# Kernel tuning notes

Measured on AMD Instinct MI355X. Metric: run time of the kernel, lower is better.

The kernel has to match this reference:

```python
import jax, jax.numpy as jnp
import numpy as np

T = 15
L = 10.0
LAM = 0.1
RHO = 1.0
NUM_CONV_A = 32
NUM_CONV_B = 32
DICT_DIM = 7
STRIDE_A = 1
STRIDE_B = 1
DN = ('NCHW', 'OIHW', 'NCHW')


def _fro_normalize(W):
    # normalize each (d, d) filter slice by its Frobenius norm (torch F.normalize, p='fro', dim=(-1,-2))
    n = jnp.sqrt(jnp.sum(W * W, axis=(-1, -2), keepdims=True))
    return W / jnp.maximum(n, 1e-12)


def _conv(y, W, s):
    # torch F.conv2d(y, W, stride=s), VALID padding
    return jax.lax.conv_general_dilated(y, W, (s, s), 'VALID', dimension_numbers=DN)


def _convT(x, W, s):
    # torch F.conv_transpose2d(x, W, stride=s); W in forward-conv layout (O, I, kh, kw)
    return jax.lax.conv_transpose(x, W, (s, s), 'VALID', dimension_numbers=DN, transpose_kernel=True)


def setup_inputs() -> dict:
    key = jax.random.key(0)
    ky, ka, kb = jax.random.split(key, 3)
    y = jax.random.normal(ky, (16, 1, 256, 256), dtype=jnp.float32)
    A = _fro_normalize(jax.random.normal(ka, (NUM_CONV_A, 1, DICT_DIM, DICT_DIM), dtype=jnp.float32))
    B = _fro_normalize(jax.random.normal(kb, (NUM_CONV_B, 1, DICT_DIM, DICT_DIM), dtype=jnp.float32))
    return {'y': y, 'A': A, 'B': B}


def reference(y, A, B):
    n, _, H, W = y.shape
    Dx = (H - DICT_DIM) // STRIDE_A + 1
    Du = (H - DICT_DIM) // STRIDE_B + 1
    Dx2 = (W - DICT_DIM) // STRIDE_A + 1
    Du2 = (W - DICT_DIM) // STRIDE_B + 1
    x0 = jnp.zeros((n, NUM_CONV_A, Dx, Dx2), dtype=y.dtype)
    u0 = jnp.zeros((n, NUM_CONV_B, Du, Du2), dtype=y.dtype)

    def step(carry, _):
        x_old, x_tmp, u_old, u_tmp, t_old = carry
        Ax = _convT((1.0 + 1.0 / RHO) * x_tmp, A, STRIDE_A)
        Bu = _convT(u_tmp, B, STRIDE_B)
        res = y - (Ax + Bu)
        x_new = x_tmp + _conv(res, A, STRIDE_A) / L
        u_new = u_tmp + _conv(res, B, STRIDE_B) / L
        # twosided soft-threshold
        u_new = jax.nn.relu(jnp.abs(u_new) - LAM / L) * jnp.sign(u_new)
        t_new = (1.0 + jnp.sqrt(1.0 + 4.0 * t_old * t_old)) / 2.0
        c = (t_old - 1.0) / t_new
        x_tmp2 = x_new + c * (x_new - x_old)
        u_tmp2 = u_new + c * (u_new - u_old)
        return (x_new, x_tmp2, u_new, u_tmp2, t_new), None

    init = (x0, x0, u0, u0, jnp.float32(1.0))
    (x_new, _, u_new, _, _), _ = jax.lax.scan(step, init, None, length=T)

    Ax_hat = _convT(x_new, A, STRIDE_A)
    Bu_hat = _convT(u_new, B, STRIDE_B)
    y_hat = Ax_hat + Bu_hat
    return y_hat, x_new, u_new, Ax_hat, Bu_hat
```

## Files before the change

### kernel.cpp

```cpp
#include <hip/hip_runtime.h>
#include <cmath>

#define NB 16
#define CC 32
#define HH 256
#define WW 256
#define DD 250
#define ALPHA 2.0f
#define INVL 0.1f
#define THR 0.01f

#define IMG_SZ (HH*WW)
#define IMG_TOT (NB*IMG_SZ)
#define FLD_SZ (DD*DD)
#define FLD_TOT ((size_t)NB*CC*FLD_SZ)

#define SRS 264
#define LRS 260

__device__ __forceinline__ float rfl(float x) {
    return __int_as_float(__builtin_amdgcn_readfirstlane(__float_as_int(x)));
}
__device__ __forceinline__ float sthr(float v) {
    float a = fabsf(v) - THR; a = a > 0.f ? a : 0.f;
    return (v > 0.f) ? a : ((v < 0.f) ? -a : 0.f);
}

#define CONV_ROW(ACC, Aa) do { \
    _Pragma("unroll") \
    for (int b = 0; b < 7; ++b) { \
        const float wv = wt[Aa][b]; \
        ACC.x += wv*win[b+0]; ACC.y += wv*win[b+1]; \
        ACC.z += wv*win[b+2]; ACC.w += wv*win[b+3]; \
    } } while (0)

#define GATH_ROW(ACC, Aa) do { \
    _Pragma("unroll") \
    for (int b = 0; b < 7; ++b) { \
        const float wv = wt[Aa][b]; \
        ACC.x += wv*win[8-b+0]; ACC.y += wv*win[8-b+1]; \
        ACC.z += wv*win[8-b+2]; ACC.w += wv*win[8-b+3]; \
    } } while (0)

__global__ __launch_bounds__(512) void k_step(
    const float* __restrict__ rin,
    const float* su_cur, float* su_on,
    float* __restrict__ Xinc, float* __restrict__ Uacc,
    const float* __restrict__ Afil, const float* __restrict__ Bfil,
    float cmom, int first)
{
    __shared__ __align__(16) float resT[22*SRS];
    __shared__ __align__(16) float stile[2][16*SRS];

    const int p0  = blockIdx.x * 16;
    const int f   = blockIdx.y;
    const int n   = blockIdx.z;
    const int tid = threadIdx.x;
    const bool isx = (f == 0);

    {
        float4 z = make_float4(0.f,0.f,0.f,0.f);
        float4* sp = (float4*)&stile[0][0];
        for (int i = tid; i < 2*16*SRS/4; i += 512) sp[i] = z;
    }
    {
        const float* rb = rin + (size_t)n * IMG_SZ;
        for (int i = tid; i < 22*66; i += 512) {
            int r  = i / 66;
            int c4 = (i - r*66) << 2;
            int gr = p0 + r;
            float4 v = make_float4(0.f,0.f,0.f,0.f);
            if (gr < HH && c4 < WW) v = *(const float4*)(rb + gr*WW + c4);
            *(float4*)&resT[r*SRS + c4] = v;
        }
    }
    __syncthreads();

    const int rg  = tid >> 6;
    const int q4  = (tid & 63) << 2;
    const bool qok = (q4 <= 248);
    const int p_0 = p0 + 2*rg;

    const float* Wb = isx ? Afil : Bfil;
    float* img = (isx ? Xinc : Uacc) + (size_t)n * IMG_SZ;

    const bool momentum = (!isx) && (!first) && (cmom != 0.f);
    const bool plain    = (!isx) && (!first) && (cmom == 0.f);

    float4 ia0 = make_float4(0.f,0.f,0.f,0.f), ia1 = ia0, ia2 = ia0;

    const size_t fbase = (size_t)n * CC * FLD_SZ;
    const bool r0ok = qok && (p_0     < DD);
    const bool r1ok = qok && (p_0 + 1 < DD);
    const size_t off0 = fbase + (size_t)p_0*DD + q4;
    const size_t off1 = off0 + DD;

    for (int c = 0; c < CC; ++c) {
        float wt[7][7];
        {
            const float* Wp = Wb + c*49;
#pragma unroll
            for (int a = 0; a < 7; ++a)
#pragma unroll
                for (int b = 0; b < 7; ++b)
                    wt[a][b] = rfl(Wp[a*7 + b]);
        }

        const size_t co = (size_t)c * FLD_SZ;
        float4 sc0 = make_float4(0.f,0.f,0.f,0.f), sc1 = sc0, so0 = sc0, so1 = sc0;
        if (momentum) {
            if (r0ok) { sc0 = *(const float4*)(su_cur + co + off0);
                        so0 = *(const float4*)(su_on  + co + off0); }
            if (r1ok) { sc1 = *(const float4*)(su_cur + co + off1);
                        so1 = *(const float4*)(su_on  + co + off1); }
        } else if (plain) {
            if (r0ok) sc0 = *(const float4*)(su_cur + co + off0);
            if (r1ok) sc1 = *(const float4*)(su_cur + co + off1);
        }

        float4 a0 = make_float4(0.f,0.f,0.f,0.f), a1 = a0;
#pragma unroll
        for (int rr = 0; rr < 8; ++rr) {
            const float* lp = &resT[(2*rg + rr)*SRS + q4];
            float4 A0 = *(const float4*)lp;
            float4 A1 = *(const float4*)(lp + 4);
            float4 A2 = *(const float4*)(lp + 8);
            const float win[12] = {A0.x,A0.y,A0.z,A0.w, A1.x,A1.y,A1.z,A1.w,
                                   A2.x,A2.y,A2.z,A2.w};
            if (rr <= 6) CONV_ROW(a0, rr);
            if (rr >= 1) CONV_ROW(a1, rr-1);
        }

        float4 o0 = make_float4(a0.x*INVL, a0.y*INVL, a0.z*INVL, a0.w*INVL);
        float4 o1 = make_float4(a1.x*INVL, a1.y*INVL, a1.z*INVL, a1.w*INVL);
        if (momentum) {
            o0.x += sc0.x + cmom*(sc0.x - so0.x);
            o0.y += sc0.y + cmom*(sc0.y - so0.y);
            o0.z += sc0.z + cmom*(sc0.z - so0.z);
            o0.w += sc0.w + cmom*(sc0.w - so0.w);
            o1.x += sc1.x + cmom*(sc1.x - so1.x);
            o1.y += sc1.y + cmom*(sc1.y - so1.y);
            o1.z += sc1.z + cmom*(sc1.z - so1.z);
            o1.w += sc1.w + cmom*(sc1.w - so1.w);
        } else if (plain) {
            o0.x += sc0.x; o0.y += sc0.y; o0.z += sc0.z; o0.w += sc0.w;
            o1.x += sc1.x; o1.y += sc1.y; o1.z += sc1.z; o1.w += sc1.w;
        }
        if (!isx) {
            o0.x = sthr(o0.x); o0.y = sthr(o0.y); o0.z = sthr(o0.z); o0.w = sthr(o0.w);
            o1.x = sthr(o1.x); o1.y = sthr(o1.y); o1.z = sthr(o1.z); o1.w = sthr(o1.w);
        }

        const int bb = c & 1;
        if (r0ok) {
            if (!isx) {
                float* dst = su_on + co + off0;
                if (q4 <= 244) *(float4*)dst = o0;
                else           *(float2*)dst = make_float2(o0.x, o0.y);
            }
            float* d0 = &stile[bb][(2*rg)*SRS + q4 + 8];
            if (q4 <= 244) *(float4*)d0 = o0;
            else           *(float2*)d0 = make_float2(o0.x, o0.y);
        }
        if (r1ok) {
            if (!isx) {
                float* dst = su_on + co + off1;
                if (q4 <= 244) *(float4*)dst = o1;
                else           *(float2*)dst = make_float2(o1.x, o1.y);
            }
            float* d1 = &stile[bb][(2*rg + 1)*SRS + q4 + 8];
            if (q4 <= 244) *(float4*)d1 = o1;
            else           *(float2*)d1 = make_float2(o1.x, o1.y);
        }
        __syncthreads();
#pragma unroll
        for (int k9 = 0; k9 < 9; ++k9) {
            const int k = 3*rg - 6 + k9;
            if (k >= 0 && k < 16) {
                const float* sp = &stile[bb][k*SRS + q4];
                float4 B0 = *(const float4*)sp;
                float4 B1 = *(const float4*)(sp + 4);
                float4 B2 = *(const float4*)(sp + 8);
                const float win[12] = {B0.x,B0.y,B0.z,B0.w, B1.x,B1.y,B1.z,B1.w,
                                       B2.x,B2.y,B2.z,B2.w};
                if (k9 <= 6)            GATH_ROW(ia0, 6 - k9);
                if (k9 >= 1 && k9 <= 7) GATH_ROW(ia1, 7 - k9);
                if (k9 >= 2)            GATH_ROW(ia2, 8 - k9);
            }
        }
    }

#pragma unroll
    for (int d = 0; d < 3; ++d) {
        const int h = 3*rg + d;
        if (h < 22) {
            const int habs = p0 + h;
            if (habs < HH) {
                float4 v = (d == 0) ? ia0 : (d == 1) ? ia1 : ia2;
                float* ip = img + (size_t)habs*WW + q4;
                if (h >= 6 && h <= 15) {
                    *(float4*)ip = v;
                } else {
                    atomicAdd(ip + 0, v.x);
                    atomicAdd(ip + 1, v.y);
                    atomicAdd(ip + 2, v.z);
                    atomicAdd(ip + 3, v.w);
                }
            }
        }
    }
}

__global__ __launch_bounds__(256) void k_res(
    const float* __restrict__ y,
    float* Xinc, float* Uacc,
    const float* __restrict__ XAv,
    float* XBv,
    float* Uc,
    float* __restrict__ resb, float* __restrict__ Racc,
    float cb, float cm, float alf)
{
    int i = blockIdx.x*256 + threadIdx.x;
    if (i >= IMG_TOT/4) return;
    float4 z = make_float4(0.f,0.f,0.f,0.f);

    float4 xi = ((const float4*)Xinc)[i];  ((float4*)Xinc)[i] = z;
    float4 ua = ((const float4*)Uacc)[i];  ((float4*)Uacc)[i] = z;
    float4 xa = ((const float4*)XAv)[i];

    float4 xt;
    if (cb != 0.f) {
        float4 xb = ((const float4*)XBv)[i];
        const float cbp = 1.f + cb;
        xt.x = cbp*xa.x - cb*xb.x + xi.x;
        xt.y = cbp*xa.y - cb*xb.y + xi.y;
        xt.z = cbp*xa.z - cb*xb.z + xi.z;
        xt.w = cbp*xa.w - cb*xb.w + xi.w;
    } else {
        xt.x = xa.x + xi.x; xt.y = xa.y + xi.y;
        xt.z = xa.z + xi.z; xt.w = xa.w + xi.w;
    }
    ((float4*)XBv)[i] = xt;

    float4 ucp = z;
    if (cm != 0.f) ucp = ((const float4*)Uc)[i];
    ((float4*)Uc)[i] = ua;

    float4 yv = ((const float4*)y)[i];
    const float cp = 1.f + cm;
    float4 r;
    r.x = yv.x - ALPHA*(cp*xt.x - cm*xa.x) - (cp*ua.x - cm*ucp.x);
    r.y = yv.y - ALPHA*(cp*xt.y - cm*xa.y) - (cp*ua.y - cm*ucp.y);
    r.z = yv.z - ALPHA*(cp*xt.z - cm*xa.z) - (cp*ua.z - cm*ucp.z);
    r.w = yv.w - ALPHA*(cp*xt.w - cm*xa.w) - (cp*ua.w - cm*ucp.w);
    ((float4*)resb)[i] = r;

    float4 ra = ((const float4*)Racc)[i];
    ra.x += alf*r.x; ra.y += alf*r.y; ra.z += alf*r.z; ra.w += alf*r.w;
    ((float4*)Racc)[i] = ra;
}

__global__ __launch_bounds__(256) void k_xfield(
    const float* __restrict__ Racc, const float* __restrict__ yimg,
    float* __restrict__ xout, const float* __restrict__ Afil, float alf0)
{
    __shared__ float lr[22*LRS + 8];

    const int c   = blockIdx.x;
    const int p0  = blockIdx.y * 16;
    const int n   = blockIdx.z;
    const int tid = threadIdx.x;

    const float* rb = Racc + (size_t)n * IMG_SZ;
    const float* yb = yimg + (size_t)n * IMG_SZ;
#pragma unroll
    for (int it = 0; it < 6; ++it) {
        int idx = tid + it*256;
        if (idx < 22*64) {
            int r = idx >> 6, c4 = (idx & 63) << 2;
            int gr = p0 + r;
            float4 v = make_float4(0.f,0.f,0.f,0.f);
            if (gr < HH) {
                float4 a = *(const float4*)(rb + gr*WW + c4);
                float4 b = *(const float4*)(yb + gr*WW + c4);
                v.x = a.x + alf0*b.x; v.y = a.y + alf0*b.y;
                v.z = a.z + alf0*b.z; v.w = a.w + alf0*b.w;
            }
            *(float4*)&lr[r*LRS + c4] = v;
        }
    }
    if (tid < 8) lr[22*LRS + tid] = 0.f;

    float wt[7][7];
    {
        const float* Wp = Afil + c*49;
#pragma unroll
        for (int a = 0; a < 7; ++a)
#pragma unroll
            for (int b = 0; b < 7; ++b)
                wt[a][b] = rfl(Wp[a*7 + b]);
    }
    __syncthreads();

    const int tq = tid & 63;
    const int pg = tid >> 6;
    const int q4 = tq << 2;

    float acc4[4][4];
#pragma unroll
    for (int k = 0; k < 4; ++k)
#pragma unroll
        for (int j = 0; j < 4; ++j) acc4[k][j] = 0.f;

#pragma unroll
    for (int rr = 0; rr < 10; ++rr) {
        const float* lp = &lr[(pg*4 + rr)*LRS + q4];
        float4 A0 = *(const float4*)lp;
        float4 A1 = *(const float4*)(lp + 4);
        float4 A2 = *(const float4*)(lp + 8);
        const float win[12] = {A0.x,A0.y,A0.z,A0.w, A1.x,A1.y,A1.z,A1.w,
                               A2.x,A2.y,A2.z,A2.w};
#pragma unroll
        for (int k = 0; k < 4; ++k) {
            const int a = rr - k;
            if (a >= 0 && a < 7) {
                float4 t = make_float4(acc4[k][0], acc4[k][1], acc4[k][2], acc4[k][3]);
                CONV_ROW(t, a);
                acc4[k][0] = t.x; acc4[k][1] = t.y; acc4[k][2] = t.z; acc4[k][3] = t.w;
            }
        }
    }

    const size_t base = ((size_t)n*CC + c) * FLD_SZ;
#pragma unroll
    for (int k = 0; k < 4; ++k) {
        int p = p0 + pg*4 + k;
        if (p < DD) {
            size_t off = base + (size_t)p*DD + q4;
            float4 o = make_float4(acc4[k][0]*INVL, acc4[k][1]*INVL,
                                   acc4[k][2]*INVL, acc4[k][3]*INVL);
            if (q4 <= 244)      *(float4*)(xout + off) = o;
            else if (q4 == 248) *(float2*)(xout + off) = make_float2(o.x, o.y);
        }
    }
}

__global__ __launch_bounds__(256) void k_zero4(float* a, float* b, float* c, float* d)
{
    int i = blockIdx.x*256 + threadIdx.x;
    if (i < IMG_TOT/4) {
        float4 z = make_float4(0.f,0.f,0.f,0.f);
        ((float4*)a)[i] = z;
        ((float4*)b)[i] = z;
        ((float4*)c)[i] = z;
        ((float4*)d)[i] = z;
    }
}

__global__ __launch_bounds__(256) void k_finale(
    const float* __restrict__ Xinc, const float* __restrict__ Uacc,
    const float* __restrict__ XA, const float* __restrict__ XB, float cb,
    float* __restrict__ axh, float* __restrict__ buh, float* __restrict__ yhat)
{
    int i = blockIdx.x*256 + threadIdx.x;
    if (i >= IMG_TOT/4) return;
    float4 xi = ((const float4*)Xinc)[i];
    float4 xa = ((const float4*)XA)[i];
    float4 xb = ((const float4*)XB)[i];
    float4 u  = ((const float4*)Uacc)[i];
    const float cbp = 1.f + cb;
    float4 xt;
    xt.x = cbp*xa.x - cb*xb.x + xi.x;
    xt.y = cbp*xa.y - cb*xb.y + xi.y;
    xt.z = cbp*xa.z - cb*xb.z + xi.z;
    xt.w = cbp*xa.w - cb*xb.w + xi.w;
    ((float4*)axh)[i] = xt;
    ((float4*)buh)[i] = u;
    float4 s = make_float4(xt.x+u.x, xt.y+u.y, xt.z+u.z, xt.w+u.w);
    ((float4*)yhat)[i] = s;
}

extern "C" void kernel_launch(void* const* d_in, const int* in_sizes, int n_in,
                              void* d_out, int out_size, void* d_ws, size_t ws_size,
                              hipStream_t stream) {
    const float* y = (const float*)d_in[0];
    const float* A = (const float*)d_in[1];
    const float* B = (const float*)d_in[2];

    float* out  = (float*)d_out;
    float* yhat = out;
    float* xout = out + IMG_TOT;
    float* uout = xout + FLD_TOT;
    float* axh  = uout + FLD_TOT;
    float* buh  = axh + IMG_TOT;

    float* ws   = (float*)d_ws;
    float* Pu0  = ws;
    float* XP0  = Pu0 + FLD_TOT;
    float* XP1  = XP0 + IMG_TOT;
    float* Uc   = XP1 + IMG_TOT;
    float* Xinc = Uc + IMG_TOT;
    float* Uacc = Xinc + IMG_TOT;
    float* Racc = Uacc + IMG_TOT;

    float* Pu[2] = {Pu0, uout};
    float* XP[2] = {XP0, XP1};
    float* res   = yhat;

    float cv[15];
    {
        float t = 1.0f;
        for (int k = 0; k < 15; ++k) {
            float tn = (1.0f + sqrtf(1.0f + 4.0f*t*t)) * 0.5f;
            cv[k] = (t - 1.0f) / tn;
            t = tn;
        }
    }
    float alpha[15];
    {
        double bp[15] = {0}, bc[15] = {0}, bn[15];
        bc[0] = 1.0;
        for (int t = 1; t < 15; ++t) {
            double cm = (double)cv[t-1];
            for (int s = 0; s < 15; ++s) bn[s] = (1.0+cm)*bc[s] - cm*bp[s];
            bn[t] += 1.0;
            for (int s = 0; s < 15; ++s) { bp[s] = bc[s]; bc[s] = bn[s]; }
        }
        for (int s = 0; s < 15; ++s) alpha[s] = (float)bc[s];
    }

    dim3 blk512(512), blk256(256);
    dim3 gS(16, 2, NB);
    int  gE = (IMG_TOT/4 + 255)/256;

    k_zero4<<<gE, blk256, 0, stream>>>(XP0, Xinc, Uacc, Racc);

    k_step<<<gS, blk512, 0, stream>>>(y, Pu[0], Pu[1], Xinc, Uacc, A, B, 0.0f, 1);

    for (int t = 1; t < 15; ++t) {
        const float cm = cv[t-1];
        const float cb = (t >= 2) ? cv[t-2] : 0.0f;
        k_res<<<gE, blk256, 0, stream>>>(y, Xinc, Uacc,
                                         XP[(t-1)&1], XP[t&1], Uc,
                                         res, Racc, cb, cm, alpha[t]);
        k_step<<<gS, blk512, 0, stream>>>(res, Pu[t&1], Pu[(t+1)&1],
                                          Xinc, Uacc, A, B, cm, 0);
    }

    k_xfield<<<dim3(CC, 16, NB), blk256, 0, stream>>>(Racc, y, xout, A, alpha[0]);
    k_finale<<<gE, blk256, 0, stream>>>(Xinc, Uacc, XP[0], XP[1], cv[13],
                                        axh, buh, yhat);
}
```

Before: 4.358 ms.

## Replace x-branch conv/convT with precomputed 13x13 autocorrelation kernel plus border fix

The x-path computes A^T A r as a single 13x13 convolution, using a kernel precomputed once from the A filters. It no longer runs a 32-channel forward conv followed by a transpose conv. VALID-boundary effects are corrected by recomputing the 6-pixel image border band exactly through a small gband/xband pass. The u-path keeps the original fused conv/convT but is split across two channel halves, one per block, each writing its own partial image. This removes most of the x-branch FLOPs and atomics, at the cost of extra kernel launches, a gbuf workspace and a two-buffer sum in k_res.

```diff
diff --git a/kernel.cpp b/kernel.cpp
--- a/kernel.cpp
+++ b/kernel.cpp
@@ -16,7 +16,10 @@
 #define FLD_TOT ((size_t)NB*CC*FLD_SZ)
 
 #define SRS 264
+#define XRS 272
 #define LRS 260
+#define GBD 5856
+#define NBAND 6000
 
 __device__ __forceinline__ float rfl(float x) {
     return __int_as_float(__builtin_amdgcn_readfirstlane(__float_as_int(x)));
@@ -42,21 +45,20 @@
         ACC.z += wv*win[8-b+2]; ACC.w += wv*win[8-b+3]; \
     } } while (0)
 
-__global__ __launch_bounds__(512) void k_step(
+__global__ __launch_bounds__(512) void k_ustep(
     const float* __restrict__ rin,
     const float* su_cur, float* su_on,
-    float* __restrict__ Xinc, float* __restrict__ Uacc,
-    const float* __restrict__ Afil, const float* __restrict__ Bfil,
+    float* __restrict__ Up0, float* __restrict__ Up1,
+    const float* __restrict__ Bfil,
     float cmom, int first)
 {
     __shared__ __align__(16) float resT[22*SRS];
     __shared__ __align__(16) float stile[2][16*SRS];
 
     const int p0  = blockIdx.x * 16;
-    const int f   = blockIdx.y;
+    const int ch0 = blockIdx.y * 16;
     const int n   = blockIdx.z;
     const int tid = threadIdx.x;
-    const bool isx = (f == 0);
 
     {
         float4 z = make_float4(0.f,0.f,0.f,0.f);
@@ -81,11 +83,9 @@
     const bool qok = (q4 <= 248);
     const int p_0 = p0 + 2*rg;
 
-    const float* Wb = isx ? Afil : Bfil;
-    float* img = (isx ? Xinc : Uacc) + (size_t)n * IMG_SZ;
-
-    const bool momentum = (!isx) && (!first) && (cmom != 0.f);
-    const bool plain    = (!isx) && (!first) && (cmom == 0.f);
+    float* img = (blockIdx.y ? Up1 : Up0) + (size_t)n * IMG_SZ;
+    const bool momentum = (!first) && (cmom != 0.f);
+    const bool plain    = (!first) && (cmom == 0.f);
 
     float4 ia0 = make_float4(0.f,0.f,0.f,0.f), ia1 = ia0, ia2 = ia0;
 
@@ -95,10 +95,11 @@
     const size_t off0 = fbase + (size_t)p_0*DD + q4;
     const size_t off1 = off0 + DD;
 
-    for (int c = 0; c < CC; ++c) {
+    for (int i16 = 0; i16 < 16; ++i16) {
+        const int c = ch0 + i16;
         float wt[7][7];
         {
-            const float* Wp = Wb + c*49;
+            const float* Wp = Bfil + c*49;
 #pragma unroll
             for (int a = 0; a < 7; ++a)
 #pragma unroll
@@ -146,33 +147,28 @@
             o0.x += sc0.x; o0.y += sc0.y; o0.z += sc0.z; o0.w += sc0.w;
             o1.x += sc1.x; o1.y += sc1.y; o1.z += sc1.z; o1.w += sc1.w;
         }
-        if (!isx) {
-            o0.x = sthr(o0.x); o0.y = sthr(o0.y); o0.z = sthr(o0.z); o0.w = sthr(o0.w);
-            o1.x = sthr(o1.x); o1.y = sthr(o1.y); o1.z = sthr(o1.z); o1.w = sthr(o1.w);
-        }
-
-        const int bb = c & 1;
+        o0.x = sthr(o0.x); o0.y = sthr(o0.y); o0.z = sthr(o0.z); o0.w = sthr(o0.w);
+        o1.x = sthr(o1.x); o1.y = sthr(o1.y); o1.z = sthr(o1.z); o1.w = sthr(o1.w);
+
+        const int bb = i16 & 1;
         if (r0ok) {
-            if (!isx) {
-                float* dst = su_on + co + off0;
-                if (q4 <= 244) *(float4*)dst = o0;
-                else           *(float2*)dst = make_float2(o0.x, o0.y);
-            }
+            float* dst = su_on + co + off0;
+            if (q4 <= 244) *(float4*)dst = o0;
+            else           *(float2*)dst = make_float2(o0.x, o0.y);
             float* d0 = &stile[bb][(2*rg)*SRS + q4 + 8];
             if (q4 <= 244) *(float4*)d0 = o0;
             else           *(float2*)d0 = make_float2(o0.x, o0.y);
         }
         if (r1ok) {
-            if (!isx) {
-                float* dst = su_on + co + off1;
-                if (q4 <= 244) *(float4*)dst = o1;
-                else           *(float2*)dst = make_float2(o1.x, o1.y);
-            }
+            float* dst = su_on + co + off1;
+            if (q4 <= 244) *(float4*)dst = o1;
+            else           *(float2*)dst = make_float2(o1.x, o1.y);
             float* d1 = &stile[bb][(2*rg + 1)*SRS + q4 + 8];
             if (q4 <= 244) *(float4*)d1 = o1;
             else           *(float2*)d1 = make_float2(o1.x, o1.y);
         }
         __syncthreads();
+
 #pragma unroll
         for (int k9 = 0; k9 < 9; ++k9) {
             const int k = 3*rg - 6 + k9;
@@ -211,9 +207,196 @@
     }
 }
 
+__global__ void k_kernA(const float* __restrict__ A, float* __restrict__ KA)
+{
+    int t = threadIdx.x;
+    if (t >= 169) return;
+    int dy = t / 13 - 6, dx = t % 13 - 6;
+    float s = 0.f;
+    for (int c = 0; c < CC; ++c) {
+        const float* Ac = A + c*49;
+        for (int a = 0; a < 7; ++a) {
+            int aa = a + dy;
+            if (aa < 0 || aa > 6) continue;
+            for (int b = 0; b < 7; ++b) {
+                int bb = b + dx;
+                if (bb < 0 || bb > 6) continue;
+                s += Ac[a*7 + b] * Ac[aa*7 + bb];
+            }
+        }
+    }
+    KA[t] = s;
+}
+
+__global__ __launch_bounds__(256) void k_xcomp(
+    const float* __restrict__ rin, float* __restrict__ Xinc,
+    const float* __restrict__ KAg)
+{
+    __shared__ __align__(16) float rt[28*XRS];
+    __shared__ float ka[169];
+
+    const int h0  = blockIdx.x * 16;
+    const int n   = blockIdx.y;
+    const int tid = threadIdx.x;
+
+    if (tid < 169) ka[tid] = KAg[tid];
+    for (int i = tid; i < 28*16; i += 256) {
+        int r = i >> 4, j = i & 15;
+        rt[r*XRS + ((j < 8) ? j : (256 + j))] = 0.f;
+    }
+    {
+        const float* rb = rin + (size_t)n * IMG_SZ;
+        for (int i = tid; i < 28*64; i += 256) {
+            int r = i >> 6, c4 = (i & 63) << 2;
+            int gr = h0 - 6 + r;
+            float4 v = make_float4(0.f,0.f,0.f,0.f);
+            if (gr >= 0 && gr < HH) v = *(const float4*)(rb + gr*WW + c4);
+            *(float4*)&rt[r*XRS + 8 + c4] = v;
+        }
+    }
+    __syncthreads();
+
+    const int tq = tid & 63;
+    const int hg = tid >> 6;
+    const int w4 = tq << 2;
+
+    float acc[4][4];
+#pragma unroll
+    for (int r = 0; r < 4; ++r)
+#pragma unroll
+        for (int j = 0; j < 4; ++j) acc[r][j] = 0.f;
+
+#pragma unroll
+    for (int k = 0; k < 16; ++k) {
+        const float* lp = &rt[(hg*4 + k)*XRS + w4];
+        float4 W0 = *(const float4*)lp;
+        float4 W1 = *(const float4*)(lp + 4);
+        float4 W2 = *(const float4*)(lp + 8);
+        float4 W3 = *(const float4*)(lp + 12);
+        float4 W4 = *(const float4*)(lp + 16);
+        const float win[20] = {W0.x,W0.y,W0.z,W0.w, W1.x,W1.y,W1.z,W1.w,
+                               W2.x,W2.y,W2.z,W2.w, W3.x,W3.y,W3.z,W3.w,
+                               W4.x,W4.y,W4.z,W4.w};
+#pragma unroll
+        for (int r = 0; r < 4; ++r) {
+            const int dyk = k - r;
+            if (dyk >= 0 && dyk <= 12) {
+                const float* kr = &ka[dyk*13];
+#pragma unroll
+                for (int dx = 0; dx < 13; ++dx) {
+                    const float kv = kr[dx];
+                    acc[r][0] += kv * win[2 + dx + 0];
+                    acc[r][1] += kv * win[2 + dx + 1];
+                    acc[r][2] += kv * win[2 + dx + 2];
+                    acc[r][3] += kv * win[2 + dx + 3];
+                }
+            }
+        }
+    }
+
+#pragma unroll
+    for (int r = 0; r < 4; ++r) {
+        const int h = h0 + hg*4 + r;
+        const size_t o = (size_t)n*IMG_SZ + (size_t)h*WW + w4;
+        *(float4*)(Xinc + o) = make_float4(acc[r][0]*INVL, acc[r][1]*INVL,
+                                           acc[r][2]*INVL, acc[r][3]*INVL);
+    }
+}
+
+__global__ __launch_bounds__(256) void k_gband(
+    const float* __restrict__ rin, float* __restrict__ gbuf,
+    const float* __restrict__ Afil)
+{
+    const int c = blockIdx.x;
+    const int n = blockIdx.y;
+    const int tid = threadIdx.x;
+    float wt[7][7];
+    {
+        const float* Wp = Afil + c*49;
+#pragma unroll
+        for (int a = 0; a < 7; ++a)
+#pragma unroll
+            for (int b = 0; b < 7; ++b)
+                wt[a][b] = rfl(Wp[a*7 + b]);
+    }
+    const float* rb = rin + (size_t)n * IMG_SZ;
+    float* gp = gbuf + ((size_t)(n*CC + c)) * GBD;
+    for (int i = tid; i < GBD; i += 256) {
+        int k, l;
+        if (i < 3000) {
+            int kk = i / 250;
+            k = (kk < 6) ? kk : 238 + kk;
+            l = i - kk*250;
+        } else {
+            int j = i - 3000;
+            int r = j / 12, cc = j - r*12;
+            k = 6 + r;
+            l = (cc < 6) ? cc : 238 + cc;
+        }
+        float s = 0.f;
+#pragma unroll
+        for (int p = 0; p < 7; ++p)
+#pragma unroll
+            for (int q = 0; q < 7; ++q)
+                s += wt[p][q] * rb[(k+p)*WW + (l+q)];
+        gp[i] = s;
+    }
+}
+
+__device__ __forceinline__ int gidx(int k, int l) {
+    if (k <= 5)   return k*250 + l;
+    if (k >= 244) return (k - 238)*250 + l;
+    return 3000 + (k - 6)*12 + ((l <= 5) ? l : l - 238);
+}
+
+__global__ __launch_bounds__(256) void k_xband(
+    const float* __restrict__ gbuf, float* __restrict__ Xinc,
+    const float* __restrict__ Afil)
+{
+    __shared__ float wA[CC*49];
+    const int n   = blockIdx.y;
+    const int tid = threadIdx.x;
+    for (int i = tid; i < CC*49; i += 256) wA[i] = Afil[i];
+    __syncthreads();
+
+    int i = blockIdx.x*256 + tid;
+    if (i >= NBAND) return;
+    int h, w;
+    if (i < 3072) {
+        int r = i >> 8;
+        h = (r < 6) ? r : 244 + r;
+        w = i & 255;
+    } else {
+        int j = i - 3072;
+        int r = j / 12, cc = j - r*12;
+        h = 6 + r;
+        w = (cc < 6) ? cc : 244 + cc;
+    }
+
+    const float* gb = gbuf + (size_t)n * CC * GBD;
+    float s = 0.f;
+    for (int c = 0; c < CC; ++c) {
+        const float* wc = &wA[c*49];
+        const float* gc = gb + (size_t)c * GBD;
+#pragma unroll
+        for (int a = 0; a < 7; ++a) {
+            int k = h - a;
+            if (k < 0 || k > 249) continue;
+#pragma unroll
+            for (int b = 0; b < 7; ++b) {
+                int l = w - b;
+                if (l < 0 || l > 249) continue;
+                s += wc[a*7 + b] * gc[gidx(k, l)];
+            }
+        }
+    }
+    Xinc[(size_t)n*IMG_SZ + (size_t)h*WW + w] = s * INVL;
+}
+
 __global__ __launch_bounds__(256) void k_res(
     const float* __restrict__ y,
-    float* Xinc, float* Uacc,
+    const float* __restrict__ Xinc,
+    float* Up0, float* Up1,
     const float* __restrict__ XAv,
     float* XBv,
     float* Uc,
@@ -224,8 +407,10 @@
     if (i >= IMG_TOT/4) return;
     float4 z = make_float4(0.f,0.f,0.f,0.f);
 
-    float4 xi = ((const float4*)Xinc)[i];  ((float4*)Xinc)[i] = z;
-    float4 ua = ((const float4*)Uacc)[i];  ((float4*)Uacc)[i] = z;
+    float4 xi = ((const float4*)Xinc)[i];
+    float4 u0 = ((const float4*)Up0)[i];  ((float4*)Up0)[i] = z;
+    float4 u1 = ((const float4*)Up1)[i];  ((float4*)Up1)[i] = z;
+    float4 ua = make_float4(u0.x+u1.x, u0.y+u1.y, u0.z+u1.z, u0.w+u1.w);
     float4 xa = ((const float4*)XAv)[i];
 
     float4 xt;
@@ -358,7 +543,8 @@
 }
 
 __global__ __launch_bounds__(256) void k_finale(
-    const float* __restrict__ Xinc, const float* __restrict__ Uacc,
+    const float* __restrict__ Xinc,
+    const float* __restrict__ Up0, const float* __restrict__ Up1,
     const float* __restrict__ XA, const float* __restrict__ XB, float cb,
     float* __restrict__ axh, float* __restrict__ buh, float* __restrict__ yhat)
 {
@@ -367,7 +553,9 @@
     float4 xi = ((const float4*)Xinc)[i];
     float4 xa = ((const float4*)XA)[i];
     float4 xb = ((const float4*)XB)[i];
-    float4 u  = ((const float4*)Uacc)[i];
+    float4 u0 = ((const float4*)Up0)[i];
+    float4 u1 = ((const float4*)Up1)[i];
+    float4 u  = make_float4(u0.x+u1.x, u0.y+u1.y, u0.z+u1.z, u0.w+u1.w);
     const float cbp = 1.f + cb;
     float4 xt;
     xt.x = cbp*xa.x - cb*xb.x + xi.x;
@@ -399,9 +587,12 @@
     float* XP0  = Pu0 + FLD_TOT;
     float* XP1  = XP0 + IMG_TOT;
     float* Uc   = XP1 + IMG_TOT;
-    float* Xinc = Uc + IMG_TOT;
-    float* Uacc = Xinc + IMG_TOT;
-    float* Racc = Uacc + IMG_TOT;
+    float* Up0  = Uc + IMG_TOT;
+    float* Up1  = Up0 + IMG_TOT;
+    float* Racc = Up1 + IMG_TOT;
+    float* Xinc = Racc + IMG_TOT;
+    float* gbuf = Xinc + IMG_TOT;
+    float* KA   = gbuf + (size_t)NB*CC*GBD;
 
     float* Pu[2] = {Pu0, uout};
     float* XP[2] = {XP0, XP1};
@@ -430,24 +621,34 @@
     }
 
     dim3 blk512(512), blk256(256);
-    dim3 gS(16, 2, NB);
+    dim3 gU(16, 2, NB);
+    dim3 gXC(16, NB);
+    dim3 gGB(CC, NB);
+    dim3 gXB((NBAND + 255)/256, NB);
     int  gE = (IMG_TOT/4 + 255)/256;
 
-    k_zero4<<<gE, blk256, 0, stream>>>(XP0, Xinc, Uacc, Racc);
-
-    k_step<<<gS, blk512, 0, stream>>>(y, Pu[0], Pu[1], Xinc, Uacc, A, B, 0.0f, 1);
+    k_zero4<<<gE, blk256, 0, stream>>>(XP0, Up0, Up1, Racc);
+    k_kernA<<<1, 256, 0, stream>>>(A, KA);
+
+    k_ustep<<<gU, blk512, 0, stream>>>(y, Pu[0], Pu[1], Up0, Up1, B, 0.0f, 1);
+    k_xcomp<<<gXC, blk256, 0, stream>>>(y, Xinc, KA);
+    k_gband<<<gGB, blk256, 0, stream>>>(y, gbuf, A);
+    k_xband<<<gXB, blk256, 0, stream>>>(gbuf, Xinc, A);
 
     for (int t = 1; t < 15; ++t) {
         const float cm = cv[t-1];
         const float cb = (t >= 2) ? cv[t-2] : 0.0f;
-        k_res<<<gE, blk256, 0, stream>>>(y, Xinc, Uacc,
+        k_res<<<gE, blk256, 0, stream>>>(y, Xinc, Up0, Up1,
                                          XP[(t-1)&1], XP[t&1], Uc,
                                          res, Racc, cb, cm, alpha[t]);
-        k_step<<<gS, blk512, 0, stream>>>(res, Pu[t&1], Pu[(t+1)&1],
-                                          Xinc, Uacc, A, B, cm, 0);
+        k_ustep<<<gU, blk512, 0, stream>>>(res, Pu[t&1], Pu[(t+1)&1],
+                                           Up0, Up1, B, cm, 0);
+        k_xcomp<<<gXC, blk256, 0, stream>>>(res, Xinc, KA);
+        k_gband<<<gGB, blk256, 0, stream>>>(res, gbuf, A);
+        k_xband<<<gXB, blk256, 0, stream>>>(gbuf, Xinc, A);
     }
 
     k_xfield<<<dim3(CC, 16, NB), blk256, 0, stream>>>(Racc, y, xout, A, alpha[0]);
-    k_finale<<<gE, blk256, 0, stream>>>(Xinc, Uacc, XP[0], XP[1], cv[13],
+    k_finale<<<gE, blk256, 0, stream>>>(Xinc, Up0, Up1, XP[0], XP[1], cv[13],
                                         axh, buh, yhat);
 }
```

New measurement: 6.502 ms. 1.49x slower.
